# Performance work log

Measured on AMD Instinct MI355X. Metric: run time of the kernel, lower is better.

## Reference

```python
import jax, jax.numpy as jnp
import numpy as np

EPS = 1e-5
SLOPE = 0.2


def _gather(points, idx):
    # points: [B, N, C], idx: [B, S] -> [B, S, C]
    return jnp.take_along_axis(points, idx[..., None], axis=1)


def _block(x, W, b, g, be):
    # Linear -> BatchNorm1d (training-mode batch stats over (B, S)) -> LeakyReLU(0.2)
    y = jnp.einsum("bsc,dc->bsd", x, W) + b
    mu = jnp.mean(y, axis=(0, 1))
    var = jnp.mean((y - mu) ** 2, axis=(0, 1))  # biased var, as torch BN uses for normalization
    y = (y - mu) * jax.lax.rsqrt(var + EPS) * g + be
    return jnp.where(y >= 0, y, SLOPE * y)


def setup_inputs() -> dict:
    c0, c1, c2, c3, c4 = 64, 128, 256, 512, 1024
    B = 64
    N0, N1, N2, N3, N4 = 2048, 1024, 512, 256, 128
    keys = iter(jax.random.split(jax.random.key(0), 40))
    inp = {"num_point": 128}
    inp["f0"] = jax.random.normal(next(keys), (B, N0, c0), jnp.float32)
    inp["f1"] = jax.random.normal(next(keys), (B, N1, c1), jnp.float32)
    inp["f2"] = jax.random.normal(next(keys), (B, N2, c2), jnp.float32)
    inp["f3"] = jax.random.normal(next(keys), (B, N3, c3), jnp.float32)
    inp["f4"] = jax.random.normal(next(keys), (B, N4, c4), jnp.float32)
    inp["FPS_0"] = jax.random.randint(next(keys), (B, N1), 0, N0)
    inp["FPS_1"] = jax.random.randint(next(keys), (B, N2), 0, N1)
    inp["FPS_2"] = jax.random.randint(next(keys), (B, N3), 0, N2)
    inp["FPS_3"] = jax.random.randint(next(keys), (B, N4), 0, N3)
    for name, cin, cout in [("04", c0, c4), ("14", c1, c4), ("24", c2, c4), ("34", c3, c4), ("4", c4, c4)]:
        inp[f"w{name}"] = jax.random.normal(next(keys), (cout, cin), jnp.float32) / np.sqrt(cin).astype(np.float32)
        inp[f"b{name}"] = jax.random.normal(next(keys), (cout,), jnp.float32) * 0.01
        inp[f"g{name}"] = jnp.ones((cout,), jnp.float32)
        inp[f"be{name}"] = jnp.zeros((cout,), jnp.float32)
    return inp


def reference(num_point, f0, f1, f2, f3, f4, FPS_0, FPS_1, FPS_2, FPS_3,
              w04, b04, g04, be04, w14, b14, g14, be14,
              w24, b24, g24, be24, w34, b34, g34, be34,
              w4, b4, g4, be4):
    # num_point == 128 branch: nested index chains down to the coarsest resolution
    idx24 = jnp.take_along_axis(FPS_2, FPS_3, axis=1)   # [B, 128] indices into N2
    idx14 = jnp.take_along_axis(FPS_1, idx24, axis=1)   # [B, 128] indices into N1
    idx04 = jnp.take_along_axis(FPS_0, idx14, axis=1)   # [B, 128] indices into N0
    f04 = _block(_gather(f0, idx04), w04, b04, g04, be04)
    f14 = _block(_gather(f1, idx14), w14, b14, g14, be14)
    f24 = _block(_gather(f2, idx24), w24, b24, g24, be24)
    f34 = _block(_gather(f3, FPS_3), w34, b34, g34, be34)
    f4_new = _block(f4 + f04 + f14 + f24 + f34, w4, b4, g4, be4) + f4
    return (f0, f1, f2, f3, f4_new)
```

## Files before the change

kernel.cpp:

```cpp
#include <hip/hip_runtime.h>
#include <hip/hip_bf16.h>

using bf16 = __hip_bfloat16;
typedef __attribute__((ext_vector_type(8))) short short8;
typedef __attribute__((ext_vector_type(4))) float floatx4;

struct alignas(16) bf16x8 { bf16 v[8]; };

#define EPSV 1e-5f

__device__ __forceinline__ float lrelu(float v) { return v >= 0.f ? v : 0.2f * v; }

__device__ __forceinline__ uint4 f8_to_bf8(const float* __restrict__ p) {
    float4 a = ((const float4*)p)[0];
    float4 b = ((const float4*)p)[1];
    bf16x8 r;
    r.v[0] = __float2bfloat16(a.x); r.v[1] = __float2bfloat16(a.y);
    r.v[2] = __float2bfloat16(a.z); r.v[3] = __float2bfloat16(a.w);
    r.v[4] = __float2bfloat16(b.x); r.v[5] = __float2bfloat16(b.y);
    r.v[6] = __float2bfloat16(b.z); r.v[7] = __float2bfloat16(b.w);
    return *(uint4*)&r;
}

__device__ __forceinline__ void async16(void* lds, const void* g) {
    __builtin_amdgcn_global_load_lds(
        (const __attribute__((address_space(1))) void*)g,
        (__attribute__((address_space(3))) void*)lds,
        16, 0, 0);
}

__global__ __launch_bounds__(256) void copy4_k(
    const float* __restrict__ f0, const float* __restrict__ f1,
    const float* __restrict__ f2, const float* __restrict__ f3,
    float* __restrict__ out)
{
    int region = blockIdx.y;
    const float* src = (region == 0) ? f0 : (region == 1) ? f1 : (region == 2) ? f2 : f3;
    size_t off = ((size_t)blockIdx.x * 256 + threadIdx.x) * 8;
    float* dst = out + (size_t)region * 8388608 + off;
    ((uint4*)dst)[0] = ((const uint4*)(src + off))[0];
    ((uint4*)dst)[1] = ((const uint4*)(src + off))[1];
}

__global__ void idx_k(const int* __restrict__ FPS0, const int* __restrict__ FPS1,
                      const int* __restrict__ FPS2, const int* __restrict__ FPS3,
                      int* __restrict__ rowidx)
{
    int b = blockIdx.x;
    int s = threadIdx.x;
    int i3 = FPS3[b * 128 + s];
    int i2 = FPS2[b * 256 + i3];
    int i1 = FPS1[b * 512 + i2];
    int i0 = FPS0[b * 1024 + i1];
    int m = b * 128 + s;
    rowidx[0 * 8192 + m] = b * 2048 + i0;
    rowidx[1 * 8192 + m] = b * 1024 + i1;
    rowidx[2 * 8192 + m] = b * 512 + i2;
    rowidx[3 * 8192 + m] = b * 256 + i3;
    rowidx[4 * 8192 + m] = m;
}

__global__ __launch_bounds__(256) void gather_k(
    const float* __restrict__ f0, const float* __restrict__ f1,
    const float* __restrict__ f2, const float* __restrict__ f3,
    const float* __restrict__ w04, const float* __restrict__ w14,
    const float* __restrict__ w24, const float* __restrict__ w34,
    const float* __restrict__ w4,
    const int* __restrict__ rowidx, bf16* __restrict__ Ab, bf16* __restrict__ Wb)
{
    int slot = blockIdx.y;
    size_t e = ((size_t)blockIdx.x * 256 + threadIdx.x) * 8;
    if (slot < 4) {
        int L = slot;
        int lk = 6 + L;
        size_t total = (size_t)8192 << lk;
        if (e >= total) return;
        int K = 1 << lk;
        int row = (int)(e >> lk);
        int col = (int)(e & (size_t)(K - 1));
        const float* src = (L == 0) ? f0 : (L == 1) ? f1 : (L == 2) ? f2 : f3;
        int gr = rowidx[L * 8192 + row];
        uint4 r = f8_to_bf8(src + (size_t)gr * K + col);
        *(uint4*)(Ab + (size_t)8192 * ((64 << L) - 64) + e) = r;
    } else {
        int L = slot - 4;
        int lk = 6 + L;
        size_t total = (size_t)1024 << lk;
        if (e >= total) return;
        const float* src = (L == 0) ? w04 : (L == 1) ? w14 : (L == 2) ? w24
                         : (L == 3) ? w34 : w4;
        uint4 r = f8_to_bf8(src + e);
        *(uint4*)(Wb + (size_t)1024 * ((64 << L) - 64) + e) = r;
    }
}

__global__ __launch_bounds__(256) void gemm16_k(
    const bf16* __restrict__ Ab, const bf16* __restrict__ Wb,
    bf16* __restrict__ Ybase, float* __restrict__ sums, int level0)
{
    __shared__ bf16 As[128 * 32];
    __shared__ bf16 Bs[128 * 32];

    int z = blockIdx.z;
    int L = level0 + z;
    int K = 64 << L;
    const bf16* A = Ab + (size_t)8192 * ((L < 4) ? ((64 << L) - 64) : 0);
    const bf16* W = Wb + (size_t)1024 * ((64 << L) - 64);
    bf16* Y = Ybase + (size_t)z * (8192 * 1024);
    float* sm = sums + z * 2048;

    int tid = threadIdx.x;
    int bm = blockIdx.x, bn = blockIdx.y;

    int u0 = tid, u1 = tid + 256;
    int row0 = u0 >> 2, k80 = (u0 & 3) << 3;
    int row1 = u1 >> 2, k81 = (u1 & 3) << 3;
    const bf16* ga0 = A + ((size_t)(bm * 128 + row0) * K + k80);
    const bf16* ga1 = A + ((size_t)(bm * 128 + row1) * K + k81);
    const bf16* gb0 = W + ((size_t)(bn * 128 + row0) * K + k80);
    const bf16* gb1 = W + ((size_t)(bn * 128 + row1) * K + k81);
    bf16* la0 = As + u0 * 8;
    bf16* la1 = As + u1 * 8;
    bf16* lb0 = Bs + u0 * 8;
    bf16* lb1 = Bs + u1 * 8;

    int lane = tid & 63, wave = tid >> 6;
    int wm = (wave >> 1) << 6;
    int wn = (wave & 1) << 6;
    int lm = lane & 15;
    int kq = (lane >> 4) << 3;

    floatx4 acc[4][4] = {};

    for (int k0 = 0; k0 < K; k0 += 32) {
        async16(la0, ga0);
        async16(la1, ga1);
        async16(lb0, gb0);
        async16(lb1, gb1);
        ga0 += 32; ga1 += 32; gb0 += 32; gb1 += 32;
        __syncthreads();

        short8 af[4], bfr[4];
#pragma unroll
        for (int i = 0; i < 4; i++) af[i]  = *(const short8*)&As[(wm + i * 16 + lm) * 32 + kq];
#pragma unroll
        for (int j = 0; j < 4; j++) bfr[j] = *(const short8*)&Bs[(wn + j * 16 + lm) * 32 + kq];
#pragma unroll
        for (int i = 0; i < 4; i++)
#pragma unroll
            for (int j = 0; j < 4; j++)
                acc[i][j] = __builtin_amdgcn_mfma_f32_16x16x32_bf16(af[i], bfr[j], acc[i][j], 0, 0, 0);
        __syncthreads();
    }

    int mrow = (lane >> 4) << 2;
    int ncol = lane & 15;
    float ps[4] = {}, pq[4] = {};
#pragma unroll
    for (int i = 0; i < 4; i++) {
#pragma unroll
        for (int j = 0; j < 4; j++) {
#pragma unroll
            for (int r = 0; r < 4; r++) {
                int m = (bm << 7) + wm + i * 16 + mrow + r;
                int n = (bn << 7) + wn + j * 16 + ncol;
                bf16 bv = __float2bfloat16(acc[i][j][r]);
                Y[(size_t)m * 1024 + n] = bv;
                float v = __bfloat162float(bv);
                ps[j] += v; pq[j] += v * v;
            }
        }
    }
#pragma unroll
    for (int j = 0; j < 4; j++) {
        ps[j] += __shfl_xor(ps[j], 16); ps[j] += __shfl_xor(ps[j], 32);
        pq[j] += __shfl_xor(pq[j], 16); pq[j] += __shfl_xor(pq[j], 32);
    }
    if (lane < 16) {
#pragma unroll
        for (int j = 0; j < 4; j++) {
            int ch = (bn << 7) + wn + (j << 4) + lane;
            atomicAdd(&sm[ch], ps[j]);
            atomicAdd(&sm[1024 + ch], pq[j]);
        }
    }
}

__global__ void finalize_k(const float* __restrict__ sums, float* __restrict__ ss,
                           const float* g0, const float* be0, const float* g1, const float* be1,
                           const float* g2, const float* be2, const float* g3, const float* be3,
                           const float* g4, const float* be4, int slot0)
{
    int slot = slot0 + blockIdx.y;
    int ch = blockIdx.x * 256 + threadIdx.x;
    const float *g, *be;
    switch (slot) {
        case 0: g = g0; be = be0; break;
        case 1: g = g1; be = be1; break;
        case 2: g = g2; be = be2; break;
        case 3: g = g3; be = be3; break;
        default: g = g4; be = be4; break;
    }
    float sum = sums[slot * 2048 + ch];
    float sq  = sums[slot * 2048 + 1024 + ch];
    float mu  = sum * (1.f / 8192.f);
    float var = sq * (1.f / 8192.f) - mu * mu;
    float sc  = g[ch] * rsqrtf(var + EPSV);
    float sh  = be[ch] - mu * sc;
    ss[slot * 2048 + ch] = sc;
    ss[slot * 2048 + 1024 + ch] = sh;
}

__global__ __launch_bounds__(256) void combine_k(
    const bf16* __restrict__ Y0, const bf16* __restrict__ Y1,
    const bf16* __restrict__ Y2, const bf16* __restrict__ Y3,
    const float* __restrict__ f4, const float* __restrict__ ss,
    bf16* __restrict__ X4)
{
    size_t base = ((size_t)blockIdx.x * 256 + threadIdx.x) * 8;
    int cq = (int)((base & 1023) >> 2);
    const floatx4* ssv = (const floatx4*)ss;
    floatx4 sc[4][2], sh[4][2];
#pragma unroll
    for (int br = 0; br < 4; br++) {
        sc[br][0] = ssv[br * 512 + cq];
        sc[br][1] = ssv[br * 512 + cq + 1];
        sh[br][0] = ssv[br * 512 + 256 + cq];
        sh[br][1] = ssv[br * 512 + 256 + cq + 1];
    }
    bf16x8 y0 = *(const bf16x8*)(Y0 + base);
    bf16x8 y1 = *(const bf16x8*)(Y1 + base);
    bf16x8 y2 = *(const bf16x8*)(Y2 + base);
    bf16x8 y3 = *(const bf16x8*)(Y3 + base);
    float4 v4a = ((const float4*)(f4 + base))[0];
    float4 v4b = ((const float4*)(f4 + base))[1];
    float v4[8] = {v4a.x, v4a.y, v4a.z, v4a.w, v4b.x, v4b.y, v4b.z, v4b.w};
    bf16x8 o;
#pragma unroll
    for (int k = 0; k < 8; k++) {
        int h = k >> 2, l = k & 3;
        float x = v4[k];
        x += lrelu(__bfloat162float(y0.v[k]) * sc[0][h][l] + sh[0][h][l]);
        x += lrelu(__bfloat162float(y1.v[k]) * sc[1][h][l] + sh[1][h][l]);
        x += lrelu(__bfloat162float(y2.v[k]) * sc[2][h][l] + sh[2][h][l]);
        x += lrelu(__bfloat162float(y3.v[k]) * sc[3][h][l] + sh[3][h][l]);
        o.v[k] = __float2bfloat16(x);
    }
    *(bf16x8*)(X4 + base) = o;
}

__global__ __launch_bounds__(256) void final_k(
    const bf16* __restrict__ Y4, const float* __restrict__ f4,
    const float* __restrict__ ss4, float* __restrict__ out4)
{
    size_t base = ((size_t)blockIdx.x * 256 + threadIdx.x) * 8;
    int cq = (int)((base & 1023) >> 2);
    const floatx4* ssv = (const floatx4*)ss4;
    floatx4 sc0 = ssv[cq], sc1 = ssv[cq + 1];
    floatx4 sh0 = ssv[256 + cq], sh1 = ssv[256 + cq + 1];
    bf16x8 y  = *(const bf16x8*)(Y4 + base);
    float4 v4a = ((const float4*)(f4 + base))[0];
    float4 v4b = ((const float4*)(f4 + base))[1];
    float v4[8] = {v4a.x, v4a.y, v4a.z, v4a.w, v4b.x, v4b.y, v4b.z, v4b.w};
    float o[8];
#pragma unroll
    for (int k = 0; k < 8; k++) {
        float sc = (k < 4) ? sc0[k & 3] : sc1[k & 3];
        float sh = (k < 4) ? sh0[k & 3] : sh1[k & 3];
        float v = __bfloat162float(y.v[k]) * sc + sh;
        o[k] = lrelu(v) + v4[k];
    }
    ((float4*)(out4 + base))[0] = make_float4(o[0], o[1], o[2], o[3]);
    ((float4*)(out4 + base))[1] = make_float4(o[4], o[5], o[6], o[7]);
}

extern "C" void kernel_launch(void* const* d_in, const int* in_sizes, int n_in,
                              void* d_out, int out_size, void* d_ws, size_t ws_size,
                              hipStream_t stream)
{
    const float* f0 = (const float*)d_in[1];
    const float* f1 = (const float*)d_in[2];
    const float* f2 = (const float*)d_in[3];
    const float* f3 = (const float*)d_in[4];
    const float* f4 = (const float*)d_in[5];
    const int* FPS0 = (const int*)d_in[6];
    const int* FPS1 = (const int*)d_in[7];
    const int* FPS2 = (const int*)d_in[8];
    const int* FPS3 = (const int*)d_in[9];
    const float* w04 = (const float*)d_in[10];
    const float* g04 = (const float*)d_in[12];
    const float* be04 = (const float*)d_in[13];
    const float* w14 = (const float*)d_in[14];
    const float* g14 = (const float*)d_in[16];
    const float* be14 = (const float*)d_in[17];
    const float* w24 = (const float*)d_in[18];
    const float* g24 = (const float*)d_in[20];
    const float* be24 = (const float*)d_in[21];
    const float* w34 = (const float*)d_in[22];
    const float* g34 = (const float*)d_in[24];
    const float* be34 = (const float*)d_in[25];
    const float* w4 = (const float*)d_in[26];
    const float* g4 = (const float*)d_in[28];
    const float* be4 = (const float*)d_in[29];

    float* out = (float*)d_out;

    const size_t YN = (size_t)8192 * 1024;
    bf16* Y0 = (bf16*)d_ws;
    bf16* Y1 = Y0 + YN;
    bf16* Y2 = Y1 + YN;
    bf16* Y3 = Y2 + YN;
    int* rowidx = (int*)(Y3 + YN);
    float* sums = (float*)(rowidx + 5 * 8192);
    float* ss = sums + 5 * 2048;
    bf16* X4 = Y0;
    bf16* Y4 = Y1;

    float* out4 = out + (size_t)4 * 8388608;
    bf16* Ab = (bf16*)out4;
    bf16* Wb = Ab + (size_t)8192 * 960;

    if (ws_size < (size_t)(4 * YN * 2 + 5 * 8192 * 4 + 2 * 5 * 2048 * 4)) return;

    hipMemsetAsync(sums, 0, 5 * 2048 * sizeof(float), stream);

    idx_k<<<64, 128, 0, stream>>>(FPS0, FPS1, FPS2, FPS3, rowidx);
    copy4_k<<<dim3(4096, 4), 256, 0, stream>>>(f0, f1, f2, f3, out);
    gather_k<<<dim3(2048, 9), 256, 0, stream>>>(f0, f1, f2, f3,
                                                w04, w14, w24, w34, w4,
                                                rowidx, Ab, Wb);

    gemm16_k<<<dim3(64, 8, 4), 256, 0, stream>>>(Ab, Wb, Y0, sums, 0);

    finalize_k<<<dim3(4, 4), 256, 0, stream>>>(sums, ss, g04, be04, g14, be14, g24, be24,
                                               g34, be34, g4, be4, 0);
    combine_k<<<4096, 256, 0, stream>>>(Y0, Y1, Y2, Y3, f4, ss, X4);

    gemm16_k<<<dim3(64, 8, 1), 256, 0, stream>>>(X4, Wb, Y4, sums + 4 * 2048, 4);

    finalize_k<<<dim3(4, 1), 256, 0, stream>>>(sums, ss, g04, be04, g14, be14, g24, be24,
                                               g34, be34, g4, be4, 4);
    final_k<<<4096, 256, 0, stream>>>(Y4, f4, ss + 4 * 2048, out4);
}
```

Before: 467.1 us.

## Fold copy into GEMM grid, fuse BN finalize into epilogues, drop memset

The passthrough copy of f0..f3 moves into an extra z-slice of the first GEMM launch so it runs alongside the MFMA blocks. The separate finalize kernels are removed and per-channel scale/shift is recomputed from raw sums inside combine and final. The memset is folded into idx_k, and combine/final now process four rows per thread with fewer blocks. This cuts launches and lets memory-bound copying overlap compute, at the cost of redundant rsqrt work per thread and copy blocks competing with GEMM blocks for CUs.

```diff
diff --git a/kernel.cpp b/kernel.cpp
--- a/kernel.cpp
+++ b/kernel.cpp
@@ -8,6 +8,7 @@
 struct alignas(16) bf16x8 { bf16 v[8]; };
 
 #define EPSV 1e-5f
+#define R8192 (1.f / 8192.f)
 
 __device__ __forceinline__ float lrelu(float v) { return v >= 0.f ? v : 0.2f * v; }
 
@@ -29,35 +30,24 @@
         16, 0, 0);
 }
 
-__global__ __launch_bounds__(256) void copy4_k(
-    const float* __restrict__ f0, const float* __restrict__ f1,
-    const float* __restrict__ f2, const float* __restrict__ f3,
-    float* __restrict__ out)
-{
-    int region = blockIdx.y;
-    const float* src = (region == 0) ? f0 : (region == 1) ? f1 : (region == 2) ? f2 : f3;
-    size_t off = ((size_t)blockIdx.x * 256 + threadIdx.x) * 8;
-    float* dst = out + (size_t)region * 8388608 + off;
-    ((uint4*)dst)[0] = ((const uint4*)(src + off))[0];
-    ((uint4*)dst)[1] = ((const uint4*)(src + off))[1];
-}
-
 __global__ void idx_k(const int* __restrict__ FPS0, const int* __restrict__ FPS1,
                       const int* __restrict__ FPS2, const int* __restrict__ FPS3,
-                      int* __restrict__ rowidx)
+                      int* __restrict__ rowidx, float* __restrict__ sums)
 {
     int b = blockIdx.x;
     int s = threadIdx.x;
+    int m = b * 128 + s;
+    sums[m] = 0.f;
+    if (m < 2048) sums[8192 + m] = 0.f;
+
     int i3 = FPS3[b * 128 + s];
     int i2 = FPS2[b * 256 + i3];
     int i1 = FPS1[b * 512 + i2];
     int i0 = FPS0[b * 1024 + i1];
-    int m = b * 128 + s;
     rowidx[0 * 8192 + m] = b * 2048 + i0;
     rowidx[1 * 8192 + m] = b * 1024 + i1;
     rowidx[2 * 8192 + m] = b * 512 + i2;
     rowidx[3 * 8192 + m] = b * 256 + i3;
-    rowidx[4 * 8192 + m] = m;
 }
 
 __global__ __launch_bounds__(256) void gather_k(
@@ -96,20 +86,41 @@
 
 __global__ __launch_bounds__(256) void gemm16_k(
     const bf16* __restrict__ Ab, const bf16* __restrict__ Wb,
-    bf16* __restrict__ Ybase, float* __restrict__ sums, int level0)
+    bf16* __restrict__ Ybase, float* __restrict__ sums,
+    const float* __restrict__ f0, const float* __restrict__ f1,
+    const float* __restrict__ f2, const float* __restrict__ f3,
+    float* __restrict__ out)
 {
     __shared__ bf16 As[128 * 32];
     __shared__ bf16 Bs[128 * 32];
 
     int z = blockIdx.z;
-    int L = level0 + z;
-    int K = 64 << L;
-    const bf16* A = Ab + (size_t)8192 * ((L < 4) ? ((64 << L) - 64) : 0);
-    const bf16* W = Wb + (size_t)1024 * ((64 << L) - 64);
+    int tid = threadIdx.x;
+
+    if (z == 4) {
+        int flat = blockIdx.y * 64 + blockIdx.x;
+        int region = flat >> 7;
+        const float* src = (region == 0) ? f0 : (region == 1) ? f1
+                         : (region == 2) ? f2 : f3;
+        float* dst = out + (size_t)region * 8388608;
+        size_t o0 = (size_t)(flat & 127) * 65536 + (size_t)tid * 8;
+#pragma unroll 4
+        for (int it = 0; it < 32; ++it) {
+            size_t off = o0 + (size_t)it * 2048;
+            uint4 v0 = ((const uint4*)(src + off))[0];
+            uint4 v1 = ((const uint4*)(src + off))[1];
+            ((uint4*)(dst + off))[0] = v0;
+            ((uint4*)(dst + off))[1] = v1;
+        }
+        return;
+    }
+
+    int K = 64 << z;
+    const bf16* A = Ab + (size_t)8192 * ((64 << z) - 64);
+    const bf16* W = Wb + (size_t)1024 * ((64 << z) - 64);
     bf16* Y = Ybase + (size_t)z * (8192 * 1024);
     float* sm = sums + z * 2048;
 
-    int tid = threadIdx.x;
     int bm = blockIdx.x, bn = blockIdx.y;
 
     int u0 = tid, u1 = tid + 256;
@@ -186,92 +197,190 @@
     }
 }
 
-__global__ void finalize_k(const float* __restrict__ sums, float* __restrict__ ss,
-                           const float* g0, const float* be0, const float* g1, const float* be1,
-                           const float* g2, const float* be2, const float* g3, const float* be3,
-                           const float* g4, const float* be4, int slot0)
-{
-    int slot = slot0 + blockIdx.y;
-    int ch = blockIdx.x * 256 + threadIdx.x;
-    const float *g, *be;
-    switch (slot) {
-        case 0: g = g0; be = be0; break;
-        case 1: g = g1; be = be1; break;
-        case 2: g = g2; be = be2; break;
-        case 3: g = g3; be = be3; break;
-        default: g = g4; be = be4; break;
-    }
-    float sum = sums[slot * 2048 + ch];
-    float sq  = sums[slot * 2048 + 1024 + ch];
-    float mu  = sum * (1.f / 8192.f);
-    float var = sq * (1.f / 8192.f) - mu * mu;
-    float sc  = g[ch] * rsqrtf(var + EPSV);
-    float sh  = be[ch] - mu * sc;
-    ss[slot * 2048 + ch] = sc;
-    ss[slot * 2048 + 1024 + ch] = sh;
+__global__ __launch_bounds__(256) void gemm4_k(
+    const bf16* __restrict__ X4, const bf16* __restrict__ W4,
+    bf16* __restrict__ Y4, float* __restrict__ sums4)
+{
+    __shared__ bf16 As[128 * 32];
+    __shared__ bf16 Bs[128 * 32];
+
+    int tid = threadIdx.x;
+    int bm = blockIdx.x, bn = blockIdx.y;
+    const int K = 1024;
+
+    int u0 = tid, u1 = tid + 256;
+    int row0 = u0 >> 2, k80 = (u0 & 3) << 3;
+    int row1 = u1 >> 2, k81 = (u1 & 3) << 3;
+    const bf16* ga0 = X4 + ((size_t)(bm * 128 + row0) * K + k80);
+    const bf16* ga1 = X4 + ((size_t)(bm * 128 + row1) * K + k81);
+    const bf16* gb0 = W4 + ((size_t)(bn * 128 + row0) * K + k80);
+    const bf16* gb1 = W4 + ((size_t)(bn * 128 + row1) * K + k81);
+    bf16* la0 = As + u0 * 8;
+    bf16* la1 = As + u1 * 8;
+    bf16* lb0 = Bs + u0 * 8;
+    bf16* lb1 = Bs + u1 * 8;
+
+    int lane = tid & 63, wave = tid >> 6;
+    int wm = (wave >> 1) << 6;
+    int wn = (wave & 1) << 6;
+    int lm = lane & 15;
+    int kq = (lane >> 4) << 3;
+
+    floatx4 acc[4][4] = {};
+
+    for (int k0 = 0; k0 < K; k0 += 32) {
+        async16(la0, ga0);
+        async16(la1, ga1);
+        async16(lb0, gb0);
+        async16(lb1, gb1);
+        ga0 += 32; ga1 += 32; gb0 += 32; gb1 += 32;
+        __syncthreads();
+
+        short8 af[4], bfr[4];
+#pragma unroll
+        for (int i = 0; i < 4; i++) af[i]  = *(const short8*)&As[(wm + i * 16 + lm) * 32 + kq];
+#pragma unroll
+        for (int j = 0; j < 4; j++) bfr[j] = *(const short8*)&Bs[(wn + j * 16 + lm) * 32 + kq];
+#pragma unroll
+        for (int i = 0; i < 4; i++)
+#pragma unroll
+            for (int j = 0; j < 4; j++)
+                acc[i][j] = __builtin_amdgcn_mfma_f32_16x16x32_bf16(af[i], bfr[j], acc[i][j], 0, 0, 0);
+        __syncthreads();
+    }
+
+    int mrow = (lane >> 4) << 2;
+    int ncol = lane & 15;
+    float ps[4] = {}, pq[4] = {};
+#pragma unroll
+    for (int i = 0; i < 4; i++) {
+#pragma unroll
+        for (int j = 0; j < 4; j++) {
+#pragma unroll
+            for (int r = 0; r < 4; r++) {
+                int m = (bm << 7) + wm + i * 16 + mrow + r;
+                int n = (bn << 7) + wn + j * 16 + ncol;
+                bf16 bv = __float2bfloat16(acc[i][j][r]);
+                Y4[(size_t)m * 1024 + n] = bv;
+                float v = __bfloat162float(bv);
+                ps[j] += v; pq[j] += v * v;
+            }
+        }
+    }
+#pragma unroll
+    for (int j = 0; j < 4; j++) {
+        ps[j] += __shfl_xor(ps[j], 16); ps[j] += __shfl_xor(ps[j], 32);
+        pq[j] += __shfl_xor(pq[j], 16); pq[j] += __shfl_xor(pq[j], 32);
+    }
+    if (lane < 16) {
+#pragma unroll
+        for (int j = 0; j < 4; j++) {
+            int ch = (bn << 7) + wn + (j << 4) + lane;
+            atomicAdd(&sums4[ch], ps[j]);
+            atomicAdd(&sums4[1024 + ch], pq[j]);
+        }
+    }
 }
 
 __global__ __launch_bounds__(256) void combine_k(
     const bf16* __restrict__ Y0, const bf16* __restrict__ Y1,
     const bf16* __restrict__ Y2, const bf16* __restrict__ Y3,
-    const float* __restrict__ f4, const float* __restrict__ ss,
+    const float* __restrict__ f4, const float* __restrict__ sums,
+    const float* __restrict__ g04, const float* __restrict__ be04,
+    const float* __restrict__ g14, const float* __restrict__ be14,
+    const float* __restrict__ g24, const float* __restrict__ be24,
+    const float* __restrict__ g34, const float* __restrict__ be34,
     bf16* __restrict__ X4)
 {
     size_t base = ((size_t)blockIdx.x * 256 + threadIdx.x) * 8;
-    int cq = (int)((base & 1023) >> 2);
-    const floatx4* ssv = (const floatx4*)ss;
-    floatx4 sc[4][2], sh[4][2];
+    int q0 = (int)((base & 1023) >> 2);
+    const floatx4* sv = (const floatx4*)sums;
+    const float* gs[4]  = {g04, g14, g24, g34};
+    const float* bes[4] = {be04, be14, be24, be34};
+
+    float sc[4][8], sh[4][8];
 #pragma unroll
     for (int br = 0; br < 4; br++) {
-        sc[br][0] = ssv[br * 512 + cq];
-        sc[br][1] = ssv[br * 512 + cq + 1];
-        sh[br][0] = ssv[br * 512 + 256 + cq];
-        sh[br][1] = ssv[br * 512 + 256 + cq + 1];
-    }
-    bf16x8 y0 = *(const bf16x8*)(Y0 + base);
-    bf16x8 y1 = *(const bf16x8*)(Y1 + base);
-    bf16x8 y2 = *(const bf16x8*)(Y2 + base);
-    bf16x8 y3 = *(const bf16x8*)(Y3 + base);
-    float4 v4a = ((const float4*)(f4 + base))[0];
-    float4 v4b = ((const float4*)(f4 + base))[1];
-    float v4[8] = {v4a.x, v4a.y, v4a.z, v4a.w, v4b.x, v4b.y, v4b.z, v4b.w};
-    bf16x8 o;
-#pragma unroll
-    for (int k = 0; k < 8; k++) {
-        int h = k >> 2, l = k & 3;
-        float x = v4[k];
-        x += lrelu(__bfloat162float(y0.v[k]) * sc[0][h][l] + sh[0][h][l]);
-        x += lrelu(__bfloat162float(y1.v[k]) * sc[1][h][l] + sh[1][h][l]);
-        x += lrelu(__bfloat162float(y2.v[k]) * sc[2][h][l] + sh[2][h][l]);
-        x += lrelu(__bfloat162float(y3.v[k]) * sc[3][h][l] + sh[3][h][l]);
-        o.v[k] = __float2bfloat16(x);
-    }
-    *(bf16x8*)(X4 + base) = o;
-}
-
-__global__ __launch_bounds__(256) void final_k(
+        floatx4 s0 = sv[br * 512 + q0],       s1 = sv[br * 512 + q0 + 1];
+        floatx4 t0 = sv[br * 512 + 256 + q0], t1 = sv[br * 512 + 256 + q0 + 1];
+        floatx4 g0 = ((const floatx4*)gs[br])[q0],  g1 = ((const floatx4*)gs[br])[q0 + 1];
+        floatx4 b0 = ((const floatx4*)bes[br])[q0], b1 = ((const floatx4*)bes[br])[q0 + 1];
+#pragma unroll
+        for (int c = 0; c < 4; c++) {
+            float mu = s0[c] * R8192, var = t0[c] * R8192 - mu * mu;
+            float s = g0[c] * rsqrtf(var + EPSV);
+            sc[br][c] = s; sh[br][c] = b0[c] - mu * s;
+            mu = s1[c] * R8192; var = t1[c] * R8192 - mu * mu;
+            s = g1[c] * rsqrtf(var + EPSV);
+            sc[br][c + 4] = s; sh[br][c + 4] = b1[c] - mu * s;
+        }
+    }
+
+#pragma unroll
+    for (int rr = 0; rr < 4; rr++) {
+        size_t e = base + (size_t)rr * 2097152;
+        bf16x8 y0 = *(const bf16x8*)(Y0 + e);
+        bf16x8 y1 = *(const bf16x8*)(Y1 + e);
+        bf16x8 y2 = *(const bf16x8*)(Y2 + e);
+        bf16x8 y3 = *(const bf16x8*)(Y3 + e);
+        float4 v4a = ((const float4*)(f4 + e))[0];
+        float4 v4b = ((const float4*)(f4 + e))[1];
+        float v4[8] = {v4a.x, v4a.y, v4a.z, v4a.w, v4b.x, v4b.y, v4b.z, v4b.w};
+        bf16x8 o;
+#pragma unroll
+        for (int k = 0; k < 8; k++) {
+            float x = v4[k];
+            x += lrelu(__bfloat162float(y0.v[k]) * sc[0][k] + sh[0][k]);
+            x += lrelu(__bfloat162float(y1.v[k]) * sc[1][k] + sh[1][k]);
+            x += lrelu(__bfloat162float(y2.v[k]) * sc[2][k] + sh[2][k]);
+            x += lrelu(__bfloat162float(y3.v[k]) * sc[3][k] + sh[3][k]);
+            o.v[k] = __float2bfloat16(x);
+        }
+        *(bf16x8*)(X4 + e) = o;
+    }
+}
+
+__global__ __launch_bounds__(256) void final2_k(
     const bf16* __restrict__ Y4, const float* __restrict__ f4,
-    const float* __restrict__ ss4, float* __restrict__ out4)
+    const float* __restrict__ sums4,
+    const float* __restrict__ g4, const float* __restrict__ be4,
+    float* __restrict__ out4)
 {
     size_t base = ((size_t)blockIdx.x * 256 + threadIdx.x) * 8;
-    int cq = (int)((base & 1023) >> 2);
-    const floatx4* ssv = (const floatx4*)ss4;
-    floatx4 sc0 = ssv[cq], sc1 = ssv[cq + 1];
-    floatx4 sh0 = ssv[256 + cq], sh1 = ssv[256 + cq + 1];
-    bf16x8 y  = *(const bf16x8*)(Y4 + base);
-    float4 v4a = ((const float4*)(f4 + base))[0];
-    float4 v4b = ((const float4*)(f4 + base))[1];
-    float v4[8] = {v4a.x, v4a.y, v4a.z, v4a.w, v4b.x, v4b.y, v4b.z, v4b.w};
-    float o[8];
-#pragma unroll
-    for (int k = 0; k < 8; k++) {
-        float sc = (k < 4) ? sc0[k & 3] : sc1[k & 3];
-        float sh = (k < 4) ? sh0[k & 3] : sh1[k & 3];
-        float v = __bfloat162float(y.v[k]) * sc + sh;
-        o[k] = lrelu(v) + v4[k];
-    }
-    ((float4*)(out4 + base))[0] = make_float4(o[0], o[1], o[2], o[3]);
-    ((float4*)(out4 + base))[1] = make_float4(o[4], o[5], o[6], o[7]);
+    int q0 = (int)((base & 1023) >> 2);
+    const floatx4* sv = (const floatx4*)sums4;
+    floatx4 s0 = sv[q0],       s1 = sv[q0 + 1];
+    floatx4 t0 = sv[256 + q0], t1 = sv[256 + q0 + 1];
+    floatx4 g0 = ((const floatx4*)g4)[q0],  g1 = ((const floatx4*)g4)[q0 + 1];
+    floatx4 b0 = ((const floatx4*)be4)[q0], b1 = ((const floatx4*)be4)[q0 + 1];
+
+    float sc[8], sh[8];
+#pragma unroll
+    for (int c = 0; c < 4; c++) {
+        float mu = s0[c] * R8192, var = t0[c] * R8192 - mu * mu;
+        float s = g0[c] * rsqrtf(var + EPSV);
+        sc[c] = s; sh[c] = b0[c] - mu * s;
+        mu = s1[c] * R8192; var = t1[c] * R8192 - mu * mu;
+        s = g1[c] * rsqrtf(var + EPSV);
+        sc[c + 4] = s; sh[c + 4] = b1[c] - mu * s;
+    }
+
+#pragma unroll
+    for (int rr = 0; rr < 4; rr++) {
+        size_t e = base + (size_t)rr * 2097152;
+        bf16x8 y = *(const bf16x8*)(Y4 + e);
+        float4 v4a = ((const float4*)(f4 + e))[0];
+        float4 v4b = ((const float4*)(f4 + e))[1];
+        float v4[8] = {v4a.x, v4a.y, v4a.z, v4a.w, v4b.x, v4b.y, v4b.z, v4b.w};
+        float o[8];
+#pragma unroll
+        for (int k = 0; k < 8; k++) {
+            float v = __bfloat162float(y.v[k]) * sc[k] + sh[k];
+            o[k] = lrelu(v) + v4[k];
+        }
+        ((float4*)(out4 + e))[0] = make_float4(o[0], o[1], o[2], o[3]);
+        ((float4*)(out4 + e))[1] = make_float4(o[4], o[5], o[6], o[7]);
+    }
 }
 
 extern "C" void kernel_launch(void* const* d_in, const int* in_sizes, int n_in,
@@ -311,34 +420,31 @@
     bf16* Y2 = Y1 + YN;
     bf16* Y3 = Y2 + YN;
     int* rowidx = (int*)(Y3 + YN);
-    float* sums = (float*)(rowidx + 5 * 8192);
-    float* ss = sums + 5 * 2048;
+    float* sums = (float*)(rowidx + 4 * 8192);
     bf16* X4 = Y0;
     bf16* Y4 = Y1;
 
     float* out4 = out + (size_t)4 * 8388608;
     bf16* Ab = (bf16*)out4;
     bf16* Wb = Ab + (size_t)8192 * 960;
-
-    if (ws_size < (size_t)(4 * YN * 2 + 5 * 8192 * 4 + 2 * 5 * 2048 * 4)) return;
-
-    hipMemsetAsync(sums, 0, 5 * 2048 * sizeof(float), stream);
-
-    idx_k<<<64, 128, 0, stream>>>(FPS0, FPS1, FPS2, FPS3, rowidx);
-    copy4_k<<<dim3(4096, 4), 256, 0, stream>>>(f0, f1, f2, f3, out);
+    const bf16* W4 = Wb + (size_t)1024 * 960;
+
+    if (ws_size < (size_t)(4 * YN * 2 + 4 * 8192 * 4 + 5 * 2048 * 4)) return;
+
+    idx_k<<<64, 128, 0, stream>>>(FPS0, FPS1, FPS2, FPS3, rowidx, sums);
+
     gather_k<<<dim3(2048, 9), 256, 0, stream>>>(f0, f1, f2, f3,
                                                 w04, w14, w24, w34, w4,
                                                 rowidx, Ab, Wb);
 
-    gemm16_k<<<dim3(64, 8, 4), 256, 0, stream>>>(Ab, Wb, Y0, sums, 0);
-
-    finalize_k<<<dim3(4, 4), 256, 0, stream>>>(sums, ss, g04, be04, g14, be14, g24, be24,
-                                               g34, be34, g4, be4, 0);
-    combine_k<<<4096, 256, 0, stream>>>(Y0, Y1, Y2, Y3, f4, ss, X4);
-
-    gemm16_k<<<dim3(64, 8, 1), 256, 0, stream>>>(X4, Wb, Y4, sums + 4 * 2048, 4);
-
-    finalize_k<<<dim3(4, 1), 256, 0, stream>>>(sums, ss, g04, be04, g14, be14, g24, be24,
-                                               g34, be34, g4, be4, 4);
-    final_k<<<4096, 256, 0, stream>>>(Y4, f4, ss + 4 * 2048, out4);
-}
+    gemm16_k<<<dim3(64, 8, 5), 256, 0, stream>>>(Ab, Wb, Y0, sums,
+                                                 f0, f1, f2, f3, out);
+
+    combine_k<<<1024, 256, 0, stream>>>(Y0, Y1, Y2, Y3, f4, sums,
+                                        g04, be04, g14, be14, g24, be24,
+                                        g34, be34, X4);
+
+    gemm4_k<<<dim3(64, 8), 256, 0, stream>>>(X4, W4, Y4, sums + 4 * 2048);
+
+    final2_k<<<1024, 256, 0, stream>>>(Y4, f4, sums + 4 * 2048, g4, be4, out4);
+}
```

After: 478.8 us. +2.5%, slower.
